# Kernel optimization log

Hardware: AMD Instinct MI355X
Metric: run time of the kernel (lower is better)

Reference implementation:

```python
import jax, jax.numpy as jnp
import numpy as np
from jax import lax

HIDDEN_CH = 32
KS = 3


def _conv(x, w):
    # x: [B, Cin, H, W], w: [Cout, Cin, k, k] -> [B, Cout, H, W] (SAME padding)
    return lax.conv_general_dilated(
        x, w, window_strides=(1, 1), padding='SAME',
        dimension_numbers=('NCHW', 'OIHW', 'NCHW'))


def _cell(x, h, gw, gb, cw, cb):
    combined = jnp.concatenate([x, h], axis=1)
    gates = jax.nn.sigmoid(_conv(combined, gw) + gb[None, :, None, None])
    r, z = jnp.split(gates, 2, axis=1)
    combined_r = jnp.concatenate([x, r * h], axis=1)
    n = jnp.tanh(_conv(combined_r, cw) + cb[None, :, None, None])
    return (1.0 - z) * h + z * n


def setup_inputs() -> dict:
    key = jax.random.key(0)
    ks = jax.random.split(key, 9)
    B, T, H, W = 8, 16, 128, 128
    hc = HIDDEN_CH
    seq = jax.random.normal(ks[0], (B, T, H, W), dtype=jnp.float32)

    def conv_init(k, cout, cin):
        fan_in = cin * KS * KS
        bound = 1.0 / np.sqrt(fan_in)
        return jax.random.uniform(k, (cout, cin, KS, KS), jnp.float32, -bound, bound)

    def bias_init(k, cout, cin):
        bound = 1.0 / np.sqrt(cin * KS * KS)
        return jax.random.uniform(k, (cout,), jnp.float32, -bound, bound)

    # Layer 0: input_ch=1, layer 1: input_ch=hc
    gw0 = conv_init(ks[1], 2 * hc, 1 + hc)
    gb0 = bias_init(ks[2], 2 * hc, 1 + hc)
    cw0 = conv_init(ks[3], hc, 1 + hc)
    cb0 = bias_init(ks[4], hc, 1 + hc)
    gw1 = conv_init(ks[5], 2 * hc, hc + hc)
    gb1 = bias_init(ks[6], 2 * hc, hc + hc)
    cw1 = conv_init(ks[7], hc, hc + hc)
    cb1 = bias_init(ks[8], hc, hc + hc)
    return {'seq': seq, 'gw0': gw0, 'gb0': gb0, 'cw0': cw0, 'cb0': cb0,
            'gw1': gw1, 'gb1': gb1, 'cw1': cw1, 'cb1': cb1}


def reference(seq, gw0, gb0, cw0, cb0, gw1, gb1, cw1, cb1):
    B, T, H, W = seq.shape
    hc = HIDDEN_CH
    h0 = jnp.zeros((B, hc, H, W), dtype=seq.dtype)
    h1 = jnp.zeros((B, hc, H, W), dtype=seq.dtype)
    # xs: [T, B, 1, H, W]
    xs = jnp.transpose(seq, (1, 0, 2, 3))[:, :, None, :, :]

    def step(carry, x_t):
        h0, h1 = carry
        h0 = _cell(x_t, h0, gw0, gb0, cw0, cb0)
        h1 = _cell(h0, h1, gw1, gb1, cw1, cb1)
        return (h0, h1), None

    (h0, h1), _ = lax.scan(step, (h0, h1), xs)
    return h1
```

## Files before the change

### kernel.cpp

```cpp
#include <hip/hip_runtime.h>


#define HH 128
#define PH 130
#define HW 16384
#define BB 8
#define TT 16

typedef _Float16 f16x8 __attribute__((ext_vector_type(8)));
typedef float f32x4 __attribute__((ext_vector_type(4)));
typedef unsigned int u32x4 __attribute__((ext_vector_type(4)));

__device__ __forceinline__ unsigned short f2h(float x){
    return __builtin_bit_cast(unsigned short, (_Float16)x);
}
__device__ __forceinline__ float h2f(unsigned short u){
    return (float)__builtin_bit_cast(_Float16, u);
}
__device__ __forceinline__ f16x8 ld_frag(const unsigned short* p){
    u32x4 v = *(const u32x4*)p;
    return __builtin_bit_cast(f16x8, v);
}
__device__ __forceinline__ f16x8 lds_frag_w(const unsigned short* base, int spix, int q){
    u32x4 v = *(const u32x4*)(base + spix * 32 + q * 8);
    return __builtin_bit_cast(f16x8, v);
}
__device__ __forceinline__ float sigmoid_f(float a){ return 1.0f / (1.0f + __expf(-a)); }
__device__ __forceinline__ float tanh_f(float a){ float e2 = __expf(2.0f * a); return 1.0f - 2.0f / (e2 + 1.0f); }
__device__ __forceinline__ unsigned int packh2(float lo, float hi){
    return (unsigned int)f2h(lo) | ((unsigned int)f2h(hi) << 16);
}

struct SmemT {
    unsigned short hs[2][13824];
    unsigned short rh[10880];
    float xt[444];
};

__device__ __forceinline__ void halo_rc10(int s, int& gr, int& gc){
    s = s > 83 ? 83 : s;
    if (s < 34)      { gr = 0;            gc = s;      }
    else if (s < 68) { gr = 9;            gc = s - 34; }
    else if (s < 76) { gr = 1 + (s - 68); gc = 0;      }
    else             { gr = 1 + (s - 76); gc = 33;     }
}

__device__ __forceinline__ f16x8 x_im2col(const float* xt, int gr, int gc, int q){
    f16x8 v;
#pragma unroll
    for (int j = 0; j < 8; ++j) {
        int k = q * 8 + j;
        float f = 0.0f;
        if (k < 9) f = xt[(gr + k / 3) * 37 + gc + k % 3];
        v[j] = (_Float16)f;
    }
    return v;
}

__device__ __forceinline__ void stage_plane12(unsigned short* slot,
    const unsigned short* __restrict__ g, int b, int pr0, int pc0)
{
    const int wv = threadIdx.x >> 6, lane = threadIdx.x & 63;
    for (int k = wv; k < 27; k += 8) {
        int chunk = k * 64 + lane;
        int pix = chunk >> 2, part = chunk & 3;
        int r = pix / 36, c = pix - r * 36;
        int pr = pr0 + r; pr = pr < 0 ? 0 : (pr > 129 ? 129 : pr);
        int pc = pc0 + c; pc = pc < 0 ? 0 : (pc > 129 ? 129 : pc);
        const unsigned short* ga = g + ((long)((b * PH + pr) * PH + pc) * 32 + part * 8);
        __builtin_amdgcn_global_load_lds(
            (const __attribute__((address_space(1))) unsigned int*)ga,
            (__attribute__((address_space(3))) unsigned int*)(slot + k * 512),
            16, 0, 0);
    }
}

__device__ __forceinline__ void stage_x12(float* xt, const float* __restrict__ seq,
                                          int b, int t, int R0, int C0)
{
    if (threadIdx.x < 444) {
        int p = threadIdx.x;
        int r = p / 37, c = p - r * 37;
        int ir = R0 - 2 + r, ic = C0 - 2 + c;
        float v = 0.0f;
        if (ir >= 0 && ir < HH && ic >= 0 && ic < HH)
            v = seq[((long)b * TT + t) * HW + ir * HH + ic];
        xt[p] = v;
    }
}

__global__ void prep_w(const float* __restrict__ w, unsigned short* __restrict__ wf,
                       int CO, int CIT, int NSTEP, int xmode)
{
    int idx = blockIdx.x * 256 + threadIdx.x;
    int total = NSTEP * CO * 32;
    if (idx >= total) return;
    int kk = idx & 31;
    int t  = idx >> 5;
    int co = t % CO;
    int s  = t / CO;
    int lco = (co & ~31) | (2 * (co & 15) + ((co >> 4) & 1));
    float v = 0.0f;
    if (xmode && s == NSTEP - 1) {
        if (kk < 9) v = w[(lco * CIT + 0) * 9 + kk];
    } else {
        int tap = s % 9;
        int cin = (s / 9) * 32 + kk + (xmode ? 1 : 0);
        v = w[(lco * CIT + cin) * 9 + tap];
    }
    wf[idx] = f2h(v);
}

template<int L, int EMIT>
__device__ __forceinline__ void cell_compute(SmemT& sm,
    unsigned short* __restrict__ Hout,
    const unsigned short* __restrict__ Wg, const float* __restrict__ bg,
    const unsigned short* __restrict__ Wc, const float* __restrict__ bc,
    float* __restrict__ out, int b, int R0, int C0)
{
    constexpr int KG = (L == 0) ? 10 : 18;
    constexpr int KC = (L == 0) ? 10 : 18;

    const int wv = threadIdx.x >> 6, lane = threadIdx.x & 63;
    const int m16 = lane & 15, q = lane >> 4;
    const unsigned short* hp = (L == 0) ? sm.hs[0] : sm.hs[1];

    f16x8 Bc[4];
#pragma unroll
    for (int ng = 0; ng < 4; ++ng)
        Bc[ng] = ld_frag(Wg + (ng * 16 + m16) * 32 + q * 8);
    f16x8 Cc[2];
#pragma unroll
    for (int ng = 0; ng < 2; ++ng)
        Cc[ng] = ld_frag(Wc + (ng * 16 + m16) * 32 + q * 8);

    __syncthreads();

    const bool HASH = (wv >= 2);
    int hgr = 0, hgc = 0;
    halo_rc10((wv - 2) * 16 + m16, hgr, hgc);

    f32x4 gI[2][4];
    f32x4 gH[2];
#pragma unroll
    for (int ng = 0; ng < 4; ++ng) {
        float bv = bg[(ng >> 1) * 32 + 2 * m16 + (ng & 1)];
#pragma unroll
        for (int mg = 0; mg < 2; ++mg) gI[mg][ng] = f32x4{bv, bv, bv, bv};
        if (ng < 2) gH[ng] = f32x4{bv, bv, bv, bv};
    }

#pragma unroll
    for (int s = 0; s < KG; ++s) {
        f16x8 Bn[4];
        if (s + 1 < KG) {
#pragma unroll
            for (int ng = 0; ng < 4; ++ng)
                Bn[ng] = ld_frag(Wg + ((s + 1) * 64 + ng * 16 + m16) * 32 + q * 8);
        }
        f16x8 AI[2], AH;
        if (L == 0 && s == 9) {
#pragma unroll
            for (int mg = 0; mg < 2; ++mg)
                AI[mg] = x_im2col(sm.xt, wv + 1, mg * 16 + 1 + m16, q);
            AH = x_im2col(sm.xt, hgr, hgc, q);
        } else {
            const int tap = (L == 0) ? s : (s % 9);
            const unsigned short* pl = (L == 1 && s >= 9) ? sm.hs[1] : sm.hs[0];
#pragma unroll
            for (int mg = 0; mg < 2; ++mg)
                AI[mg] = lds_frag_w(pl, (wv + 1 + tap / 3) * 36 + mg * 16 + 1 + m16 + tap % 3, q);
            AH = lds_frag_w(pl, (hgr + tap / 3) * 36 + hgc + tap % 3, q);
        }
#pragma unroll
        for (int mg = 0; mg < 2; ++mg)
#pragma unroll
            for (int ng = 0; ng < 4; ++ng)
                gI[mg][ng] = __builtin_amdgcn_mfma_f32_16x16x32_f16(AI[mg], Bc[ng], gI[mg][ng], 0, 0, 0);
        if (HASH) {
#pragma unroll
            for (int ng = 0; ng < 2; ++ng)
                gH[ng] = __builtin_amdgcn_mfma_f32_16x16x32_f16(AH, Bc[ng], gH[ng], 0, 0, 0);
        }
        if (s + 1 < KG) {
#pragma unroll
            for (int ng = 0; ng < 4; ++ng) Bc[ng] = Bn[ng];
        }
    }

    unsigned int zpk[2][4];
#pragma unroll
    for (int mg = 0; mg < 2; ++mg)
#pragma unroll
        for (int rg = 0; rg < 4; ++rg) {
            int gr = wv + 1, gc = mg * 16 + 1 + q * 4 + rg;
            zpk[mg][rg] = packh2(sigmoid_f(gI[mg][2][rg]), sigmoid_f(gI[mg][3][rg]));
            float rv0 = sigmoid_f(gI[mg][0][rg]);
            float rv1 = sigmoid_f(gI[mg][1][rg]);
            unsigned int hvp = *(const unsigned int*)(hp + ((gr + 1) * 36 + gc + 1) * 32 + 2 * m16);
            float h0 = h2f((unsigned short)hvp), h1 = h2f((unsigned short)(hvp >> 16));
            *(unsigned int*)(sm.rh + (gr * 34 + gc) * 32 + 2 * m16) = packh2(rv0 * h0, rv1 * h1);
        }
    if (HASH) {
#pragma unroll
        for (int rg = 0; rg < 4; ++rg) {
            int gr, gc; halo_rc10((wv - 2) * 16 + q * 4 + rg, gr, gc);
            float rv0 = sigmoid_f(gH[0][rg]);
            float rv1 = sigmoid_f(gH[1][rg]);
            unsigned int hvp = *(const unsigned int*)(hp + ((gr + 1) * 36 + gc + 1) * 32 + 2 * m16);
            float h0 = h2f((unsigned short)hvp), h1 = h2f((unsigned short)(hvp >> 16));
            *(unsigned int*)(sm.rh + (gr * 34 + gc) * 32 + 2 * m16) = packh2(rv0 * h0, rv1 * h1);
        }
    }
    __syncthreads();

    f32x4 cacc[2][2];
#pragma unroll
    for (int mg = 0; mg < 2; ++mg)
#pragma unroll
        for (int ng = 0; ng < 2; ++ng) {
            float bv = bc[2 * m16 + ng];
            cacc[mg][ng] = f32x4{bv, bv, bv, bv};
        }
#pragma unroll
    for (int s = 0; s < KC; ++s) {
        f16x8 Cn[2];
        if (s + 1 < KC) {
#pragma unroll
            for (int ng = 0; ng < 2; ++ng)
                Cn[ng] = ld_frag(Wc + ((s + 1) * 32 + ng * 16 + m16) * 32 + q * 8);
        }
        f16x8 A2[2];
        if (L == 0 && s == 9) {
#pragma unroll
            for (int mg = 0; mg < 2; ++mg)
                A2[mg] = x_im2col(sm.xt, wv + 1, mg * 16 + 1 + m16, q);
        } else if (L == 1 && s < 9) {
#pragma unroll
            for (int mg = 0; mg < 2; ++mg)
                A2[mg] = lds_frag_w(sm.hs[0], (wv + 1 + s / 3) * 36 + mg * 16 + m16 + 1 + s % 3, q);
        } else {
            const int tap = (L == 0) ? s : (s - 9);
#pragma unroll
            for (int mg = 0; mg < 2; ++mg)
                A2[mg] = lds_frag_w(sm.rh, (wv + tap / 3) * 34 + mg * 16 + m16 + tap % 3, q);
        }
#pragma unroll
        for (int mg = 0; mg < 2; ++mg)
#pragma unroll
            for (int ng = 0; ng < 2; ++ng)
                cacc[mg][ng] = __builtin_amdgcn_mfma_f32_16x16x32_f16(A2[mg], Cc[ng], cacc[mg][ng], 0, 0, 0);
        if (s + 1 < KC) {
#pragma unroll
            for (int ng = 0; ng < 2; ++ng) Cc[ng] = Cn[ng];
        }
    }

    unsigned int hvout[2][4];
#pragma unroll
    for (int mg = 0; mg < 2; ++mg)
#pragma unroll
        for (int rg = 0; rg < 4; ++rg) {
            int lcol = mg * 16 + q * 4 + rg;
            float nv0 = tanh_f(cacc[mg][0][rg]);
            float nv1 = tanh_f(cacc[mg][1][rg]);
            float zz0 = h2f((unsigned short)zpk[mg][rg]);
            float zz1 = h2f((unsigned short)(zpk[mg][rg] >> 16));
            unsigned int hop = *(const unsigned int*)(hp + ((wv + 2) * 36 + lcol + 2) * 32 + 2 * m16);
            float ho0 = h2f((unsigned short)hop), ho1 = h2f((unsigned short)(hop >> 16));
            float hn0 = (1.0f - zz0) * ho0 + zz0 * nv0;
            float hn1 = (1.0f - zz1) * ho1 + zz1 * nv1;
            if (!EMIT) {
                long psp = (long)(b * PH + R0 + wv + 1) * PH + (C0 + lcol + 1);
                *(unsigned int*)(Hout + psp * 32 + 2 * m16) = packh2(hn0, hn1);
            } else {
                hvout[mg][rg] = packh2(hn0, hn1);
            }
        }

    if (EMIT) {
        __syncthreads();
        unsigned short* scr = sm.rh;
#pragma unroll
        for (int mg = 0; mg < 2; ++mg)
#pragma unroll
            for (int rg = 0; rg < 4; ++rg)
                *(unsigned int*)(scr + ((wv * 32 + mg * 16 + q * 4 + rg) * 32) + 2 * m16)
                    = hvout[mg][rg];
        __syncthreads();
        const int tid = threadIdx.x;
        const int rowid = tid >> 1, half = tid & 1;
        const int n = rowid >> 3, wr = rowid & 7;
        long obase = ((long)(b * 32 + n) * HH + (R0 + wr)) * HH + C0 + half * 16;
#pragma unroll
        for (int j = 0; j < 16; ++j)
            out[obase + j] = h2f(scr[(wr * 32 + half * 16 + j) * 32 + n]);
    }
}

__global__ __launch_bounds__(512, 4)
void cell_l0(const unsigned short* __restrict__ Hin, unsigned short* __restrict__ Hout,
             const float* __restrict__ seq, int t,
             const unsigned short* __restrict__ Wg, const float* __restrict__ bg,
             const unsigned short* __restrict__ Wc, const float* __restrict__ bc)
{
    __shared__ __align__(16) SmemT sm;
    const int wg = blockIdx.x;
    const int b = wg >> 6, tr = (wg >> 2) & 15, tc = wg & 3;
    const int R0 = tr * 8, C0 = tc * 32;
    stage_x12(sm.xt, seq, b, t, R0, C0);
    stage_plane12(sm.hs[0], Hin, b, R0 - 1, C0 - 1);
    cell_compute<0, 0>(sm, Hout, Wg, bg, Wc, bc, (float*)0, b, R0, C0);
}

__global__ __launch_bounds__(512, 4)
void step_pair(const unsigned short* __restrict__ h1r, unsigned short* __restrict__ h1w,
               const unsigned short* __restrict__ h0r, unsigned short* __restrict__ h0w,
               const float* __restrict__ seq, int tnext,
               const unsigned short* __restrict__ WG0, const float* __restrict__ gb0,
               const unsigned short* __restrict__ WC0, const float* __restrict__ cb0,
               const unsigned short* __restrict__ WG1, const float* __restrict__ gb1,
               const unsigned short* __restrict__ WC1, const float* __restrict__ cb1)
{
    __shared__ __align__(16) SmemT sm;
    const int wg = blockIdx.x;
    const int b = wg >> 6, tr = (wg >> 2) & 15, tc = wg & 3;
    const int R0 = tr * 8, C0 = tc * 32;
    if (blockIdx.z == 0) {
        stage_plane12(sm.hs[0], h0r, b, R0 - 1, C0 - 1);
        stage_plane12(sm.hs[1], h1r, b, R0 - 1, C0 - 1);
        cell_compute<1, 0>(sm, h1w, WG1, gb1, WC1, cb1, (float*)0, b, R0, C0);
    } else {
        stage_x12(sm.xt, seq, b, tnext, R0, C0);
        stage_plane12(sm.hs[0], h0r, b, R0 - 1, C0 - 1);
        cell_compute<0, 0>(sm, h0w, WG0, gb0, WC0, cb0, (float*)0, b, R0, C0);
    }
}

__global__ __launch_bounds__(512, 4)
void cell_l1_emit(const unsigned short* __restrict__ Hin,
                  const unsigned short* __restrict__ Xin,
                  const unsigned short* __restrict__ Wg, const float* __restrict__ bg,
                  const unsigned short* __restrict__ Wc, const float* __restrict__ bc,
                  float* __restrict__ out)
{
    __shared__ __align__(16) SmemT sm;
    const int wg = blockIdx.x;
    const int b = wg >> 6, tr = (wg >> 2) & 15, tc = wg & 3;
    const int R0 = tr * 8, C0 = tc * 32;
    stage_plane12(sm.hs[0], Xin, b, R0 - 1, C0 - 1);
    stage_plane12(sm.hs[1], Hin, b, R0 - 1, C0 - 1);
    cell_compute<1, 1>(sm, (unsigned short*)0, Wg, bg, Wc, bc, out, b, R0, C0);
}

extern "C" void kernel_launch(void* const* d_in, const int* in_sizes, int n_in,
                              void* d_out, int out_size, void* d_ws, size_t ws_size,
                              hipStream_t stream)
{
    const float* seq = (const float*)d_in[0];
    const float* gw0 = (const float*)d_in[1];
    const float* gb0 = (const float*)d_in[2];
    const float* cw0 = (const float*)d_in[3];
    const float* cb0 = (const float*)d_in[4];
    const float* gw1 = (const float*)d_in[5];
    const float* gb1 = (const float*)d_in[6];
    const float* cw1 = (const float*)d_in[7];
    const float* cb1 = (const float*)d_in[8];
    float* out = (float*)d_out;

    const size_t NSP = (size_t)BB * PH * PH * 32;

    char* p = (char*)d_ws;
    unsigned short* S0A = (unsigned short*)p; p += NSP * 2;
    unsigned short* S0B = (unsigned short*)p; p += NSP * 2;
    unsigned short* S1A = (unsigned short*)p; p += NSP * 2;
    unsigned short* S1B = (unsigned short*)p; p += NSP * 2;
    unsigned short* WG0 = (unsigned short*)p; p += 20480 * 2;
    unsigned short* WC0 = (unsigned short*)p; p += 10240 * 2;
    unsigned short* WG1 = (unsigned short*)p; p += 36864 * 2;
    unsigned short* WC1 = (unsigned short*)p; p += 18432 * 2;

    hipMemsetAsync(S0A, 0, 4 * NSP * 2, stream);

    prep_w<<<(10 * 64 * 32 + 255) / 256, 256, 0, stream>>>(gw0, WG0, 64, 33, 10, 1);
    prep_w<<<(10 * 32 * 32 + 255) / 256, 256, 0, stream>>>(cw0, WC0, 32, 33, 10, 1);
    prep_w<<<(18 * 64 * 32 + 255) / 256, 256, 0, stream>>>(gw1, WG1, 64, 64, 18, 0);
    prep_w<<<(18 * 32 * 32 + 255) / 256, 256, 0, stream>>>(cw1, WC1, 32, 64, 18, 0);

    dim3 grid1(512, 1, 1), grid2(512, 1, 2), block(512);

    cell_l0<<<grid1, block, 0, stream>>>(S0A, S0B, seq, 0, WG0, gb0, WC0, cb0);

    unsigned short *h0r = S0B, *h0w = S0A, *h1r = S1A, *h1w = S1B;
    for (int t = 0; t < TT - 1; ++t) {
        step_pair<<<grid2, block, 0, stream>>>(h1r, h1w, h0r, h0w, seq, t + 1,
                                               WG0, gb0, WC0, cb0,
                                               WG1, gb1, WC1, cb1);
        unsigned short* tmp;
        tmp = h0r; h0r = h0w; h0w = tmp;
        tmp = h1r; h1r = h1w; h1w = tmp;
    }
    cell_l1_emit<<<grid1, block, 0, stream>>>(h1r, h0r, WG1, gb1, WC1, cb1, out);
}
```

Before: 972.9 us.

## Read activation fragments from global, stage weights via double-buffered LDS

Drops the LDS staging of the padded hidden/input planes and instead loads im2col A-fragments straight from global (L2/L1 cached) memory. Weights are repacked into the MFMA fragment layout and streamed into small double-buffered LDS slots, with a block barrier per tap step. This shrinks shared memory so occupancy can rise (launch bounds raised to 6 blocks), at the cost of repeated global loads for overlapping halo reads and an added barrier on every K step.

```diff
diff --git a/kernel.cpp b/kernel.cpp
--- a/kernel.cpp
+++ b/kernel.cpp
@@ -31,8 +31,19 @@
     return (unsigned int)f2h(lo) | ((unsigned int)f2h(hi) << 16);
 }
 
+template<int CLAMP>
+__device__ __forceinline__ f16x8 gfrag(const unsigned short* __restrict__ g,
+                                       int b, int pr, int pc, int q){
+    if (CLAMP) {
+        pr = pr < 0 ? 0 : (pr > PH - 1 ? PH - 1 : pr);
+        pc = pc < 0 ? 0 : (pc > PH - 1 ? PH - 1 : pc);
+    }
+    return ld_frag(g + (long)((b * PH + pr) * PH + pc) * 32 + q * 8);
+}
+
 struct SmemT {
-    unsigned short hs[2][13824];
+    unsigned short wg[2][2048];
+    unsigned short wc[2][1024];
     unsigned short rh[10880];
     float xt[444];
 };
@@ -55,24 +66,6 @@
         v[j] = (_Float16)f;
     }
     return v;
-}
-
-__device__ __forceinline__ void stage_plane12(unsigned short* slot,
-    const unsigned short* __restrict__ g, int b, int pr0, int pc0)
-{
-    const int wv = threadIdx.x >> 6, lane = threadIdx.x & 63;
-    for (int k = wv; k < 27; k += 8) {
-        int chunk = k * 64 + lane;
-        int pix = chunk >> 2, part = chunk & 3;
-        int r = pix / 36, c = pix - r * 36;
-        int pr = pr0 + r; pr = pr < 0 ? 0 : (pr > 129 ? 129 : pr);
-        int pc = pc0 + c; pc = pc < 0 ? 0 : (pc > 129 ? 129 : pc);
-        const unsigned short* ga = g + ((long)((b * PH + pr) * PH + pc) * 32 + part * 8);
-        __builtin_amdgcn_global_load_lds(
-            (const __attribute__((address_space(1))) unsigned int*)ga,
-            (__attribute__((address_space(3))) unsigned int*)(slot + k * 512),
-            16, 0, 0);
-    }
 }
 
 __device__ __forceinline__ void stage_x12(float* xt, const float* __restrict__ seq,
@@ -95,10 +88,15 @@
     int idx = blockIdx.x * 256 + threadIdx.x;
     int total = NSTEP * CO * 32;
     if (idx >= total) return;
-    int kk = idx & 31;
-    int t  = idx >> 5;
-    int co = t % CO;
-    int s  = t / CO;
+    int j  = idx & 7;
+    int t  = idx >> 3;
+    int l  = t & 63;
+    int t2 = t >> 6;
+    int NG = CO >> 4;
+    int ng = t2 % NG;
+    int s  = t2 / NG;
+    int co = ng * 16 + (l & 15);
+    int kk = (l >> 4) * 8 + j;
     int lco = (co & ~31) | (2 * (co & 15) + ((co >> 4) & 1));
     float v = 0.0f;
     if (xmode && s == NSTEP - 1) {
@@ -113,6 +111,8 @@
 
 template<int L, int EMIT>
 __device__ __forceinline__ void cell_compute(SmemT& sm,
+    const unsigned short* __restrict__ Xp,
+    const unsigned short* __restrict__ Hp,
     unsigned short* __restrict__ Hout,
     const unsigned short* __restrict__ Wg, const float* __restrict__ bg,
     const unsigned short* __restrict__ Wc, const float* __restrict__ bc,
@@ -121,19 +121,15 @@
     constexpr int KG = (L == 0) ? 10 : 18;
     constexpr int KC = (L == 0) ? 10 : 18;
 
-    const int wv = threadIdx.x >> 6, lane = threadIdx.x & 63;
+    const int tid = threadIdx.x;
+    const int wv = tid >> 6, lane = tid & 63;
     const int m16 = lane & 15, q = lane >> 4;
-    const unsigned short* hp = (L == 0) ? sm.hs[0] : sm.hs[1];
-
-    f16x8 Bc[4];
-#pragma unroll
-    for (int ng = 0; ng < 4; ++ng)
-        Bc[ng] = ld_frag(Wg + (ng * 16 + m16) * 32 + q * 8);
-    f16x8 Cc[2];
-#pragma unroll
-    for (int ng = 0; ng < 2; ++ng)
-        Cc[ng] = ld_frag(Wc + (ng * 16 + m16) * 32 + q * 8);
-
+    const int tid4 = tid * 4, tid2 = tid * 2, lane8 = lane * 8;
+
+    *(unsigned long long*)(sm.wg[0] + tid4) =
+        *(const unsigned long long*)(Wg + tid4);
+    unsigned long long wng =
+        *(const unsigned long long*)(Wg + 2048 + tid4);
     __syncthreads();
 
     const bool HASH = (wv >= 2);
@@ -152,11 +148,10 @@
 
 #pragma unroll
     for (int s = 0; s < KG; ++s) {
-        f16x8 Bn[4];
         if (s + 1 < KG) {
-#pragma unroll
-            for (int ng = 0; ng < 4; ++ng)
-                Bn[ng] = ld_frag(Wg + ((s + 1) * 64 + ng * 16 + m16) * 32 + q * 8);
+            *(unsigned long long*)(sm.wg[(s + 1) & 1] + tid4) = wng;
+            if (s + 2 < KG)
+                wng = *(const unsigned long long*)(Wg + (s + 2) * 2048 + tid4);
         }
         f16x8 AI[2], AH;
         if (L == 0 && s == 9) {
@@ -166,26 +161,29 @@
             AH = x_im2col(sm.xt, hgr, hgc, q);
         } else {
             const int tap = (L == 0) ? s : (s % 9);
-            const unsigned short* pl = (L == 1 && s >= 9) ? sm.hs[1] : sm.hs[0];
+            const unsigned short* pl = (L == 1 && s < 9) ? Xp : Hp;
 #pragma unroll
             for (int mg = 0; mg < 2; ++mg)
-                AI[mg] = lds_frag_w(pl, (wv + 1 + tap / 3) * 36 + mg * 16 + 1 + m16 + tap % 3, q);
-            AH = lds_frag_w(pl, (hgr + tap / 3) * 36 + hgc + tap % 3, q);
-        }
+                AI[mg] = gfrag<0>(pl, b, R0 + wv + tap / 3,
+                                  C0 + mg * 16 + m16 + tap % 3, q);
+            AH = gfrag<1>(pl, b, R0 - 1 + hgr + tap / 3,
+                          C0 - 1 + hgc + tap % 3, q);
+        }
+        f16x8 Bf[4];
+#pragma unroll
+        for (int ng = 0; ng < 4; ++ng)
+            Bf[ng] = ld_frag(sm.wg[s & 1] + ng * 512 + lane8);
 #pragma unroll
         for (int mg = 0; mg < 2; ++mg)
 #pragma unroll
             for (int ng = 0; ng < 4; ++ng)
-                gI[mg][ng] = __builtin_amdgcn_mfma_f32_16x16x32_f16(AI[mg], Bc[ng], gI[mg][ng], 0, 0, 0);
+                gI[mg][ng] = __builtin_amdgcn_mfma_f32_16x16x32_f16(AI[mg], Bf[ng], gI[mg][ng], 0, 0, 0);
         if (HASH) {
 #pragma unroll
             for (int ng = 0; ng < 2; ++ng)
-                gH[ng] = __builtin_amdgcn_mfma_f32_16x16x32_f16(AH, Bc[ng], gH[ng], 0, 0, 0);
-        }
-        if (s + 1 < KG) {
-#pragma unroll
-            for (int ng = 0; ng < 4; ++ng) Bc[ng] = Bn[ng];
-        }
+                gH[ng] = __builtin_amdgcn_mfma_f32_16x16x32_f16(AH, Bf[ng], gH[ng], 0, 0, 0);
+        }
+        if (s + 1 < KG) __syncthreads();
     }
 
     unsigned int zpk[2][4];
@@ -197,7 +195,8 @@
             zpk[mg][rg] = packh2(sigmoid_f(gI[mg][2][rg]), sigmoid_f(gI[mg][3][rg]));
             float rv0 = sigmoid_f(gI[mg][0][rg]);
             float rv1 = sigmoid_f(gI[mg][1][rg]);
-            unsigned int hvp = *(const unsigned int*)(hp + ((gr + 1) * 36 + gc + 1) * 32 + 2 * m16);
+            unsigned int hvp = *(const unsigned int*)(
+                Hp + (long)((b * PH + R0 + gr) * PH + C0 + gc) * 32 + 2 * m16);
             float h0 = h2f((unsigned short)hvp), h1 = h2f((unsigned short)(hvp >> 16));
             *(unsigned int*)(sm.rh + (gr * 34 + gc) * 32 + 2 * m16) = packh2(rv0 * h0, rv1 * h1);
         }
@@ -207,11 +206,15 @@
             int gr, gc; halo_rc10((wv - 2) * 16 + q * 4 + rg, gr, gc);
             float rv0 = sigmoid_f(gH[0][rg]);
             float rv1 = sigmoid_f(gH[1][rg]);
-            unsigned int hvp = *(const unsigned int*)(hp + ((gr + 1) * 36 + gc + 1) * 32 + 2 * m16);
+            unsigned int hvp = *(const unsigned int*)(
+                Hp + (long)((b * PH + R0 + gr) * PH + C0 + gc) * 32 + 2 * m16);
             float h0 = h2f((unsigned short)hvp), h1 = h2f((unsigned short)(hvp >> 16));
             *(unsigned int*)(sm.rh + (gr * 34 + gc) * 32 + 2 * m16) = packh2(rv0 * h0, rv1 * h1);
         }
     }
+
+    *(unsigned int*)(sm.wc[0] + tid2) = *(const unsigned int*)(Wc + tid2);
+    unsigned int wnc = *(const unsigned int*)(Wc + 1024 + tid2);
     __syncthreads();
 
     f32x4 cacc[2][2];
@@ -224,11 +227,10 @@
         }
 #pragma unroll
     for (int s = 0; s < KC; ++s) {
-        f16x8 Cn[2];
         if (s + 1 < KC) {
-#pragma unroll
-            for (int ng = 0; ng < 2; ++ng)
-                Cn[ng] = ld_frag(Wc + ((s + 1) * 32 + ng * 16 + m16) * 32 + q * 8);
+            *(unsigned int*)(sm.wc[(s + 1) & 1] + tid2) = wnc;
+            if (s + 2 < KC)
+                wnc = *(const unsigned int*)(Wc + (s + 2) * 1024 + tid2);
         }
         f16x8 A2[2];
         if (L == 0 && s == 9) {
@@ -238,22 +240,24 @@
         } else if (L == 1 && s < 9) {
 #pragma unroll
             for (int mg = 0; mg < 2; ++mg)
-                A2[mg] = lds_frag_w(sm.hs[0], (wv + 1 + s / 3) * 36 + mg * 16 + m16 + 1 + s % 3, q);
+                A2[mg] = gfrag<0>(Xp, b, R0 + wv + s / 3,
+                                  C0 + mg * 16 + m16 + s % 3, q);
         } else {
             const int tap = (L == 0) ? s : (s - 9);
 #pragma unroll
             for (int mg = 0; mg < 2; ++mg)
                 A2[mg] = lds_frag_w(sm.rh, (wv + tap / 3) * 34 + mg * 16 + m16 + tap % 3, q);
         }
+        f16x8 Cf[2];
+#pragma unroll
+        for (int ng = 0; ng < 2; ++ng)
+            Cf[ng] = ld_frag(sm.wc[s & 1] + ng * 512 + lane8);
 #pragma unroll
         for (int mg = 0; mg < 2; ++mg)
 #pragma unroll
             for (int ng = 0; ng < 2; ++ng)
-                cacc[mg][ng] = __builtin_amdgcn_mfma_f32_16x16x32_f16(A2[mg], Cc[ng], cacc[mg][ng], 0, 0, 0);
-        if (s + 1 < KC) {
-#pragma unroll
-            for (int ng = 0; ng < 2; ++ng) Cc[ng] = Cn[ng];
-        }
+                cacc[mg][ng] = __builtin_amdgcn_mfma_f32_16x16x32_f16(A2[mg], Cf[ng], cacc[mg][ng], 0, 0, 0);
+        if (s + 1 < KC) __syncthreads();
     }
 
     unsigned int hvout[2][4];
@@ -266,7 +270,8 @@
             float nv1 = tanh_f(cacc[mg][1][rg]);
             float zz0 = h2f((unsigned short)zpk[mg][rg]);
             float zz1 = h2f((unsigned short)(zpk[mg][rg] >> 16));
-            unsigned int hop = *(const unsigned int*)(hp + ((wv + 2) * 36 + lcol + 2) * 32 + 2 * m16);
+            unsigned int hop = *(const unsigned int*)(
+                Hp + (long)((b * PH + R0 + wv + 1) * PH + C0 + lcol + 1) * 32 + 2 * m16);
             float ho0 = h2f((unsigned short)hop), ho1 = h2f((unsigned short)(hop >> 16));
             float hn0 = (1.0f - zz0) * ho0 + zz0 * nv0;
             float hn1 = (1.0f - zz1) * ho1 + zz1 * nv1;
@@ -288,7 +293,6 @@
                 *(unsigned int*)(scr + ((wv * 32 + mg * 16 + q * 4 + rg) * 32) + 2 * m16)
                     = hvout[mg][rg];
         __syncthreads();
-        const int tid = threadIdx.x;
         const int rowid = tid >> 1, half = tid & 1;
         const int n = rowid >> 3, wr = rowid & 7;
         long obase = ((long)(b * 32 + n) * HH + (R0 + wr)) * HH + C0 + half * 16;
@@ -298,7 +302,7 @@
     }
 }
 
-__global__ __launch_bounds__(512, 4)
+__global__ __launch_bounds__(512, 6)
 void cell_l0(const unsigned short* __restrict__ Hin, unsigned short* __restrict__ Hout,
              const float* __restrict__ seq, int t,
              const unsigned short* __restrict__ Wg, const float* __restrict__ bg,
@@ -309,11 +313,11 @@
     const int b = wg >> 6, tr = (wg >> 2) & 15, tc = wg & 3;
     const int R0 = tr * 8, C0 = tc * 32;
     stage_x12(sm.xt, seq, b, t, R0, C0);
-    stage_plane12(sm.hs[0], Hin, b, R0 - 1, C0 - 1);
-    cell_compute<0, 0>(sm, Hout, Wg, bg, Wc, bc, (float*)0, b, R0, C0);
-}
-
-__global__ __launch_bounds__(512, 4)
+    cell_compute<0, 0>(sm, (const unsigned short*)0, Hin, Hout,
+                       Wg, bg, Wc, bc, (float*)0, b, R0, C0);
+}
+
+__global__ __launch_bounds__(512, 6)
 void step_pair(const unsigned short* __restrict__ h1r, unsigned short* __restrict__ h1w,
                const unsigned short* __restrict__ h0r, unsigned short* __restrict__ h0w,
                const float* __restrict__ seq, int tnext,
@@ -327,17 +331,16 @@
     const int b = wg >> 6, tr = (wg >> 2) & 15, tc = wg & 3;
     const int R0 = tr * 8, C0 = tc * 32;
     if (blockIdx.z == 0) {
-        stage_plane12(sm.hs[0], h0r, b, R0 - 1, C0 - 1);
-        stage_plane12(sm.hs[1], h1r, b, R0 - 1, C0 - 1);
-        cell_compute<1, 0>(sm, h1w, WG1, gb1, WC1, cb1, (float*)0, b, R0, C0);
+        cell_compute<1, 0>(sm, h0r, h1r, h1w,
+                           WG1, gb1, WC1, cb1, (float*)0, b, R0, C0);
     } else {
         stage_x12(sm.xt, seq, b, tnext, R0, C0);
-        stage_plane12(sm.hs[0], h0r, b, R0 - 1, C0 - 1);
-        cell_compute<0, 0>(sm, h0w, WG0, gb0, WC0, cb0, (float*)0, b, R0, C0);
-    }
-}
-
-__global__ __launch_bounds__(512, 4)
+        cell_compute<0, 0>(sm, (const unsigned short*)0, h0r, h0w,
+                           WG0, gb0, WC0, cb0, (float*)0, b, R0, C0);
+    }
+}
+
+__global__ __launch_bounds__(512, 6)
 void cell_l1_emit(const unsigned short* __restrict__ Hin,
                   const unsigned short* __restrict__ Xin,
                   const unsigned short* __restrict__ Wg, const float* __restrict__ bg,
@@ -348,9 +351,8 @@
     const int wg = blockIdx.x;
     const int b = wg >> 6, tr = (wg >> 2) & 15, tc = wg & 3;
     const int R0 = tr * 8, C0 = tc * 32;
-    stage_plane12(sm.hs[0], Xin, b, R0 - 1, C0 - 1);
-    stage_plane12(sm.hs[1], Hin, b, R0 - 1, C0 - 1);
-    cell_compute<1, 1>(sm, (unsigned short*)0, Wg, bg, Wc, bc, out, b, R0, C0);
+    cell_compute<1, 1>(sm, Xin, Hin, (unsigned short*)0,
+                       Wg, bg, Wc, bc, out, b, R0, C0);
 }
 
 extern "C" void kernel_launch(void* const* d_in, const int* in_sizes, int n_in,
```

Measured after the change: 2.301 ms. 136% more time.
